# Kernel tuning notes

Measured on AMD Instinct MI355X. Metric: run time of the kernel, lower is better.

The kernel has to match this reference:

```python
import jax, jax.numpy as jnp
import numpy as np

N_PATCHES = 16
PATCH = 128
RECEPTIVE_FIELD = 0


def setup_inputs() -> dict:
    key = jax.random.key(0)
    k1, k2, k3, k4 = jax.random.split(key, 4)
    B, C = 8, 3
    Hl = Wl = 256
    Hh = Wh = 2048
    x_low = jax.random.normal(k1, (B, C, Hl, Wl), jnp.float32)
    x_high = jax.random.normal(k2, (B, C, Hh, Wh), jnp.float32)
    # attention must be strictly positive (log is taken)
    attention = jax.random.uniform(k3, (B, Hl, Wl), jnp.float32, minval=1e-3, maxval=1.0)
    # uniform noise for the Gumbel-max trick (torch.rand_like equivalent)
    noise_u = jax.random.uniform(k4, (B, Hl * Wl), jnp.float32, minval=1e-6, maxval=1.0 - 1e-6)
    return {"x_low": x_low, "x_high": x_high, "attention": attention, "noise_u": noise_u}


def reference(x_low, x_high, attention, noise_u):
    B, Ha, Wa = attention.shape
    # --- Gumbel-max top-k sampling without replacement ---
    logits = jnp.log(attention).reshape(B, -1)          # [B, Ha*Wa]
    z = -jnp.log(-jnp.log(noise_u))                     # Gumbel noise
    _, idx = jax.lax.top_k(logits + z, N_PATCHES)       # [B, N] flat indices
    sampled_attention = jnp.take_along_axis(attention.reshape(B, -1), idx, axis=1)  # [B, N]
    # unravel flat indices -> (row, col) in sample space
    samples = jnp.stack([idx // Wa, idx % Wa], axis=-1).astype(jnp.float32)  # [B, N, 2]

    # --- offset computation (FromTensors.patches) ---
    Hl, Wl = x_low.shape[2], x_low.shape[3]
    Hh, Wh = x_high.shape[2], x_high.shape[3]
    scale_offsets = jnp.array([Hh / Hl, Wh / Wl], jnp.float32)
    prev_patch = jnp.array([Hl - RECEPTIVE_FIELD, Wl - RECEPTIVE_FIELD], jnp.float32)
    steps = prev_patch * scale_offsets / jnp.array([Ha, Wa], jnp.float32)
    patch_f = jnp.array([PATCH, PATCH], jnp.float32)
    base_off = 0.0 if RECEPTIVE_FIELD <= 0 else RECEPTIVE_FIELD / 2.0
    offsets = jnp.round(base_off * scale_offsets + samples * steps + steps / 2.0 - patch_f / 2.0).astype(jnp.int32)  # [B, N, 2]

    # --- patch extraction with zero padding of patch_size//2 ---
    pad_const = PATCH // 2
    img = jnp.pad(x_high, ((0, 0), (0, 0), (pad_const, pad_const), (pad_const, pad_const)))  # [B,C,Hh+P,Wh+P]
    offsets = offsets + pad_const
    C = img.shape[1]

    def crop(img_b, off):  # img_b: [C,H,W], off: [2]
        return jax.lax.dynamic_slice(img_b, (0, off[0], off[1]), (C, PATCH, PATCH))

    patches = jax.vmap(lambda im, offs: jax.vmap(lambda o: crop(im, o))(offs))(img, offsets)  # [B,N,C,P,P]
    return patches, sampled_attention
```

## Files before the change

kernel.cpp:

```cpp
#include <hip/hip_runtime.h>

typedef unsigned long long u64;
typedef unsigned int u32;

#define HW 65536
#define NSPLIT 64
#define CHUNK (HW / NSPLIT)
#define PERLANE (CHUNK / 64)
#define NSEL 16
#define NB 8
#define NPATCH 16
#define NC 3
#define HH 2048
#define PATCHSZ 128

__device__ __forceinline__ u32 f2o(float f) {
  u32 u = __float_as_uint(f);
  return (u & 0x80000000u) ? ~u : (u | 0x80000000u);
}

__device__ __forceinline__ u64 wave_max64(u64 k) {
#pragma unroll
  for (int off = 1; off < 64; off <<= 1) {
    u32 lo = __shfl_xor((u32)k, off, 64);
    u32 hi = __shfl_xor((u32)(k >> 32), off, 64);
    u64 o = ((u64)hi << 32) | lo;
    if (o > k) k = o;
  }
  return k;
}

__global__ __launch_bounds__(64) void scan_topk(
    const float* __restrict__ att, const float* __restrict__ noise,
    u64* __restrict__ cand) {
  const int blk = blockIdx.x;
  const int b = blk >> 6;
  const int s = blk & (NSPLIT - 1);
  const int lane = threadIdx.x;
  const int ebase = s * CHUNK;
  const float* ab = att + b * HW + ebase;
  const float* nb = noise + b * HW + ebase;

  u64 keys[NSEL];
#pragma unroll
  for (int i = 0; i < NSEL; i++) keys[i] = 0ULL;

#pragma unroll
  for (int k = 0; k < PERLANE; k++) {
    const int off = lane + (k << 6);
    float a = ab[off];
    float u = nb[off];
    float key = logf(a) - logf(-logf(u));
    u32 e = (u32)(ebase + off);
    u64 kk = ((u64)f2o(key) << 32) | (0xFFFFFFFFu - e);
#pragma unroll
    for (int i = 0; i < NSEL; i++) {
      if (kk > keys[i]) { u64 t = keys[i]; keys[i] = kk; kk = t; }
    }
  }

  u64 won = 0ULL;
#pragma unroll
  for (int r = 0; r < NSEL; r++) {
    u64 g = wave_max64(keys[0]);
    if (lane == r) won = g;
    if (keys[0] == g) {
#pragma unroll
      for (int i = 0; i < NSEL - 1; i++) keys[i] = keys[i + 1];
      keys[NSEL - 1] = 0ULL;
    }
  }
  if (lane < NSEL) cand[blk * NSEL + lane] = won;
}

__global__ __launch_bounds__(64) void merge_topk(
    const u64* __restrict__ cand, const float* __restrict__ att,
    int* __restrict__ idx_sel, float* __restrict__ att_out) {
  const int b = blockIdx.x;
  const int lane = threadIdx.x;
  const u64* cb = cand + b * (NSPLIT * NSEL);

  u64 keys[NSEL];
#pragma unroll
  for (int i = 0; i < NSEL; i++) keys[i] = 0ULL;

#pragma unroll
  for (int k = 0; k < 16; k++) {
    u64 kk = cb[lane + (k << 6)];
#pragma unroll
    for (int i = 0; i < NSEL; i++) {
      if (kk > keys[i]) { u64 t = keys[i]; keys[i] = kk; kk = t; }
    }
  }

  u64 won = 0ULL;
#pragma unroll
  for (int r = 0; r < NSEL; r++) {
    u64 g = wave_max64(keys[0]);
    if (lane == r) won = g;
    if (keys[0] == g) {
#pragma unroll
      for (int i = 0; i < NSEL - 1; i++) keys[i] = keys[i + 1];
      keys[NSEL - 1] = 0ULL;
    }
  }
  if (lane < NSEL) {
    u32 e = 0xFFFFFFFFu - (u32)(won & 0xFFFFFFFFu);
    idx_sel[b * NSEL + lane] = (int)e;
    att_out[b * NSEL + lane] = att[b * HW + (int)e];
  }
}

__global__ __launch_bounds__(256) void patch_extract(
    const float* __restrict__ xh, const int* __restrict__ idx_sel,
    float* __restrict__ out) {
  const int blk = blockIdx.x;
  const int h = blk & 1;
  const int pairc = blk >> 1;
  const int c = pairc % 3;
  const int bn = pairc / 3;
  const int b = bn >> 4;
  const int e = idx_sel[bn];
  const int sr = e >> 8;
  const int sc = e & 255;
  const int r0 = sr * 8 - 60 + h * 64;
  const int c0 = sc * 8 - 60;
  const float* src = xh + ((size_t)(b * NC + c) << 22);
  float* dst = out + (size_t)pairc * (PATCHSZ * PATCHSZ) + (size_t)h * (64 * PATCHSZ);

#pragma unroll
  for (int i = threadIdx.x; i < 64 * 32; i += 256) {
    const int pr = i >> 5;
    const int q = i & 31;
    const int r = r0 + pr;
    const int cc = c0 + (q << 2);
    float4 v = make_float4(0.f, 0.f, 0.f, 0.f);
    if ((u32)r < (u32)HH && (u32)cc < (u32)HH) {
      v = *reinterpret_cast<const float4*>(src + ((size_t)r << 11) + cc);
    }
    *reinterpret_cast<float4*>(dst + ((size_t)i << 2)) = v;
  }
}

extern "C" void kernel_launch(void* const* d_in, const int* in_sizes, int n_in,
                              void* d_out, int out_size, void* d_ws, size_t ws_size,
                              hipStream_t stream) {
  (void)in_sizes; (void)n_in; (void)out_size; (void)ws_size;
  const float* x_high = (const float*)d_in[1];
  const float* att    = (const float*)d_in[2];
  const float* noise  = (const float*)d_in[3];
  float* out = (float*)d_out;
  float* att_out = out + (size_t)NB * NPATCH * NC * PATCHSZ * PATCHSZ;

  u64* cand   = (u64*)d_ws;
  int* idx_sel = (int*)((char*)d_ws + (size_t)NB * NSPLIT * NSEL * sizeof(u64));

  scan_topk<<<NB * NSPLIT, 64, 0, stream>>>(att, noise, cand);
  merge_topk<<<NB, 64, 0, stream>>>(cand, att, idx_sel, att_out);
  patch_extract<<<NB * NPATCH * NC * 2, 256, 0, stream>>>(x_high, idx_sel, out);
}
```

Before: 33.58 us.

## Replace per-chunk top-k insertion with threshold filter using chunk maxima

Measured after the change: 33.08 us. About the same (-1.5%).

```diff
diff --git a/kernel.cpp b/kernel.cpp
--- a/kernel.cpp
+++ b/kernel.cpp
@@ -4,19 +4,28 @@
 typedef unsigned int u32;
 
 #define HW 65536
-#define NSPLIT 64
-#define CHUNK (HW / NSPLIT)
-#define PERLANE (CHUNK / 64)
+#define NB 8
 #define NSEL 16
-#define NB 8
 #define NPATCH 16
 #define NC 3
 #define HH 2048
 #define PATCHSZ 128
+#define NCHUNK 256
+#define CAP 1024
 
-__device__ __forceinline__ u32 f2o(float f) {
-  u32 u = __float_as_uint(f);
-  return (u & 0x80000000u) ? ~u : (u | 0x80000000u);
+__device__ __forceinline__ u32 wkey(float a, float u) {
+  float v = __builtin_amdgcn_logf(u);
+  float w = a * __builtin_amdgcn_rcpf(-v);
+  return __float_as_uint(w);
+}
+
+__device__ __forceinline__ u32 wave_max_u32(u32 k) {
+#pragma unroll
+  for (int off = 1; off < 64; off <<= 1) {
+    u32 o = __shfl_xor(k, off, 64);
+    k = (o > k) ? o : k;
+  }
+  return k;
 }
 
 __device__ __forceinline__ u64 wave_max64(u64 k) {
@@ -30,66 +39,86 @@
   return k;
 }
 
-__global__ __launch_bounds__(64) void scan_topk(
+__global__ __launch_bounds__(256) void scan_max(
     const float* __restrict__ att, const float* __restrict__ noise,
+    u32* __restrict__ cmax, u32* __restrict__ cnt) {
+  const int b = blockIdx.x >> 6;
+  const int blk = blockIdx.x & 63;
+  const int wave = threadIdx.x >> 6;
+  const int lane = threadIdx.x & 63;
+  const int base = b * HW + blk * 1024 + wave * 256;
+
+  u32 best = 0;
+#pragma unroll
+  for (int k = 0; k < 4; k++) {
+    const int i = base + (k << 6) + lane;
+    best = max(best, wkey(att[i], noise[i]));
+  }
+  best = wave_max_u32(best);
+  if (lane == 0) cmax[b * NCHUNK + (blk << 2) + wave] = best;
+  if (blockIdx.x == 0 && threadIdx.x < NB) cnt[threadIdx.x] = 0;
+}
+
+__global__ __launch_bounds__(256) void filter(
+    const float* __restrict__ att, const float* __restrict__ noise,
+    const u32* __restrict__ cmax, u32* __restrict__ cnt,
     u64* __restrict__ cand) {
-  const int blk = blockIdx.x;
-  const int b = blk >> 6;
-  const int s = blk & (NSPLIT - 1);
+  const int b = blockIdx.x >> 6;
+  const int blk = blockIdx.x & 63;
+  const int lane = threadIdx.x & 63;
+
+  u32 k4[4];
+#pragma unroll
+  for (int j = 0; j < 4; j++) {
+    u32 v = cmax[b * NCHUNK + (j << 6) + lane];
+    k4[j] = v;
+#pragma unroll
+    for (int i = 3; i > 0; i--) {
+      if (i <= j && k4[i] > k4[i - 1]) { u32 t = k4[i - 1]; k4[i - 1] = k4[i]; k4[i] = t; }
+    }
+  }
+  u32 T = 0;
+#pragma unroll
+  for (int r = 0; r < NSEL; r++) {
+    u32 g = wave_max_u32(k4[0]);
+    T = g;
+    if (k4[0] == g) { k4[0] = k4[1]; k4[1] = k4[2]; k4[2] = k4[3]; k4[3] = 0; }
+  }
+
+  const int ebase = b * HW + blk * 1024;
+#pragma unroll
+  for (int k = 0; k < 4; k++) {
+    const int off = blk * 1024 + (k << 8) + threadIdx.x;
+    const int i = b * HW + (off - blk * 1024) + blk * 1024;
+    (void)i;
+    const int gi = ebase + (k << 8) + threadIdx.x;
+    u32 w = wkey(att[gi], noise[gi]);
+    if (w >= T) {
+      u32 pos = atomicAdd(&cnt[b], 1u);
+      if (pos < CAP) {
+        u32 e = (u32)(gi - b * HW);
+        cand[b * CAP + pos] = ((u64)w << 32) | (0xFFFFFFFFu - e);
+      }
+    }
+  }
+}
+
+__global__ __launch_bounds__(64) void final_topk(
+    const u64* __restrict__ cand, const u32* __restrict__ cnt,
+    const float* __restrict__ att, int* __restrict__ idx_sel,
+    float* __restrict__ att_out) {
+  const int b = blockIdx.x;
   const int lane = threadIdx.x;
-  const int ebase = s * CHUNK;
-  const float* ab = att + b * HW + ebase;
-  const float* nb = noise + b * HW + ebase;
+  int n = (int)cnt[b]; if (n > CAP) n = CAP;
 
   u64 keys[NSEL];
 #pragma unroll
   for (int i = 0; i < NSEL; i++) keys[i] = 0ULL;
-
+  for (int i = lane; i < n; i += 64) {
+    u64 kk = cand[b * CAP + i];
 #pragma unroll
-  for (int k = 0; k < PERLANE; k++) {
-    const int off = lane + (k << 6);
-    float a = ab[off];
-    float u = nb[off];
-    float key = logf(a) - logf(-logf(u));
-    u32 e = (u32)(ebase + off);
-    u64 kk = ((u64)f2o(key) << 32) | (0xFFFFFFFFu - e);
-#pragma unroll
-    for (int i = 0; i < NSEL; i++) {
-      if (kk > keys[i]) { u64 t = keys[i]; keys[i] = kk; kk = t; }
-    }
-  }
-
-  u64 won = 0ULL;
-#pragma unroll
-  for (int r = 0; r < NSEL; r++) {
-    u64 g = wave_max64(keys[0]);
-    if (lane == r) won = g;
-    if (keys[0] == g) {
-#pragma unroll
-      for (int i = 0; i < NSEL - 1; i++) keys[i] = keys[i + 1];
-      keys[NSEL - 1] = 0ULL;
-    }
-  }
-  if (lane < NSEL) cand[blk * NSEL + lane] = won;
-}
-
-__global__ __launch_bounds__(64) void merge_topk(
-    const u64* __restrict__ cand, const float* __restrict__ att,
-    int* __restrict__ idx_sel, float* __restrict__ att_out) {
-  const int b = blockIdx.x;
-  const int lane = threadIdx.x;
-  const u64* cb = cand + b * (NSPLIT * NSEL);
-
-  u64 keys[NSEL];
-#pragma unroll
-  for (int i = 0; i < NSEL; i++) keys[i] = 0ULL;
-
-#pragma unroll
-  for (int k = 0; k < 16; k++) {
-    u64 kk = cb[lane + (k << 6)];
-#pragma unroll
-    for (int i = 0; i < NSEL; i++) {
-      if (kk > keys[i]) { u64 t = keys[i]; keys[i] = kk; kk = t; }
+    for (int j = 0; j < NSEL; j++) {
+      if (kk > keys[j]) { u64 t = keys[j]; keys[j] = kk; kk = t; }
     }
   }
 
@@ -152,10 +181,14 @@
   float* out = (float*)d_out;
   float* att_out = out + (size_t)NB * NPATCH * NC * PATCHSZ * PATCHSZ;
 
-  u64* cand   = (u64*)d_ws;
-  int* idx_sel = (int*)((char*)d_ws + (size_t)NB * NSPLIT * NSEL * sizeof(u64));
+  char* ws = (char*)d_ws;
+  u32* cmax    = (u32*)ws;
+  u32* cnt     = (u32*)(ws + 8 * NCHUNK * 4);
+  u64* cand    = (u64*)(ws + 8 * NCHUNK * 4 + 256);
+  int* idx_sel = (int*)(ws + 8 * NCHUNK * 4 + 256 + (size_t)NB * CAP * 8);
 
-  scan_topk<<<NB * NSPLIT, 64, 0, stream>>>(att, noise, cand);
-  merge_topk<<<NB, 64, 0, stream>>>(cand, att, idx_sel, att_out);
+  scan_max<<<NB * 64, 256, 0, stream>>>(att, noise, cmax, cnt);
+  filter<<<NB * 64, 256, 0, stream>>>(att, noise, cmax, cnt, cand);
+  final_topk<<<NB, 64, 0, stream>>>(cand, cnt, att, idx_sel, att_out);
   patch_extract<<<NB * NPATCH * NC * 2, 256, 0, stream>>>(x_high, idx_sel, out);
 }
```
